# Optimization experiments

Measured on AMD Instinct MI355X. Metric: run time of the kernel, lower is better.

Reference implementation:

```python
import jax, jax.numpy as jnp
import numpy as np

NUM_EXPERTS = 8
TOP_K = 2
ROUTE_SCALE = 1.0
DIM = 1024
HID = 1024
B, S = 2, 4096


def setup_inputs() -> dict:
    key = jax.random.key(0)
    ks = jax.random.split(key, 9)
    sc = 0.05
    return {
        "x": jax.random.normal(ks[0], (B, S, DIM), dtype=jnp.float32),
        "gate_w": jax.random.normal(ks[1], (NUM_EXPERTS, DIM), dtype=jnp.float32) * sc,
        "w1": jax.random.normal(ks[2], (NUM_EXPERTS, HID, DIM), dtype=jnp.float32) * sc,
        "w2": jax.random.normal(ks[3], (NUM_EXPERTS, DIM, HID), dtype=jnp.float32) * sc,
        "w3": jax.random.normal(ks[4], (NUM_EXPERTS, HID, DIM), dtype=jnp.float32) * sc,
        "sw1": jax.random.normal(ks[5], (HID, DIM), dtype=jnp.float32) * sc,
        "sw2": jax.random.normal(ks[6], (DIM, HID), dtype=jnp.float32) * sc,
        "sw3": jax.random.normal(ks[7], (HID, DIM), dtype=jnp.float32) * sc,
        "expert_bias": jnp.zeros((NUM_EXPERTS,), dtype=jnp.float32),
    }


def reference(x, gate_w, w1, w2, w3, sw1, sw2, sw3, expert_bias):
    bs, slen, dim = x.shape
    xf = x.reshape(-1, dim)                      # [T, D]

    # ---- router (sigmoid scoring, top-k over scores + bias, gather true scores) ----
    scores = jax.nn.sigmoid((xf @ gate_w.T).astype(jnp.float32))   # [T, E]
    _, sel = jax.lax.top_k(scores + expert_bias[None, :], TOP_K)    # [T, K] int32
    top_scores = jnp.take_along_axis(scores, sel, axis=1) * ROUTE_SCALE  # [T, K]

    # ---- stable sort token-slots by chosen expert (dispatch permutation) ----
    flat_sel = sel.reshape(-1)                       # [T*K]
    order = jnp.argsort(flat_sel, stable=True)       # [T*K]
    scores_sorted = top_scores.reshape(-1)[order]    # [T*K]
    tok_idx = order // TOP_K                         # source token per slot
    expert_ids = flat_sel[order]                     # sorted expert id per slot

    routed = xf[tok_idx]                             # gather [T*K, D]
    # score_before_experts=True: scale inputs by routing score
    routed = (routed.astype(jnp.float32) * scores_sorted[:, None]).astype(x.dtype)

    # ---- grouped expert GLU MLP (loop over fixed expert count, masked) ----
    out_r = jnp.zeros_like(routed)
    for e in range(NUM_EXPERTS):
        m = (expert_ids == e)[:, None]
        h = jax.nn.silu(routed @ w1[e].T) * (routed @ w3[e].T)   # [T*K, H]
        out_r = out_r + jnp.where(m, h @ w2[e].T, jnp.zeros((), routed.dtype))

    # ---- shared expert on all tokens ----
    shared = (jax.nn.silu(xf @ sw1.T) * (xf @ sw3.T)) @ sw2.T    # [T, D]

    # NOTE: original code multiplies by routing scores again after experts
    # (in addition to score_before_experts) -- replicated faithfully.
    out_r = (out_r.astype(jnp.float32) * scores_sorted[:, None]).astype(x.dtype)

    out = shared.at[tok_idx].add(out_r)              # scatter-add combine
    return out.reshape(bs, slen, dim)
```

## Files before the change

### kernel.cpp

```cpp
#include <hip/hip_runtime.h>
#include <stdint.h>

typedef unsigned short u16;
typedef unsigned int u32;

#define T_TOK 8192
#define DIMSZ 1024
#define HIDSZ 1024
#define NE 8
#define NSLOT (T_TOK * 2)
#define NPAD (NSLOT + 1024)

typedef __attribute__((ext_vector_type(8))) __bf16 bf16x8;
typedef __attribute__((ext_vector_type(4))) float f32x4;

__device__ __forceinline__ size_t ablk(int pos, int c) {
  return ((((size_t)(pos >> 7) * 32 + (c >> 5)) * 4 + ((c >> 3) & 3)) * 128 +
          (pos & 127)) * 8 + (c & 7);
}

__device__ __forceinline__ u16 f2bf(float f) {
  u32 u = __builtin_bit_cast(u32, f);
  u += 0x7FFFu + ((u >> 16) & 1u);
  return (u16)(u >> 16);
}
__device__ __forceinline__ float bflo(u32 v) { return __builtin_bit_cast(float, v << 16); }
__device__ __forceinline__ float bfhi(u32 v) { return __builtin_bit_cast(float, v & 0xffff0000u); }
__device__ __forceinline__ u32 pack2(float a, float b) {
  return (u32)f2bf(a) | ((u32)f2bf(b) << 16);
}
__device__ __forceinline__ float silu_f(float v) { return v / (1.f + expf(-v)); }

__global__ __launch_bounds__(256) void convert_blocked(
    const float* __restrict__ s0, const float* __restrict__ s1,
    const float* __restrict__ s2, u16* __restrict__ d0, u16* __restrict__ d1,
    u16* __restrict__ d2) {
  const float* s = (blockIdx.y == 0) ? s0 : (blockIdx.y == 1) ? s1 : s2;
  u16* d = (blockIdx.y == 0) ? d0 : (blockIdx.y == 1) ? d1 : d2;
  __shared__ u16 lt[2048];
  int t = blockIdx.x;
  int rt = t >> 5, kt = t & 31;
  const float* sp = s + (size_t)rt * 64 * 1024 + kt * 32;
  int nl = threadIdx.x >> 2, k0 = (threadIdx.x & 3) * 8;
  float4 a = *(const float4*)(sp + (size_t)nl * 1024 + k0);
  float4 b = *(const float4*)(sp + (size_t)nl * 1024 + k0 + 4);
  uint4 p;
  p.x = pack2(a.x, a.y); p.y = pack2(a.z, a.w);
  p.z = pack2(b.x, b.y); p.w = pack2(b.z, b.w);
  *(uint4*)&lt[(threadIdx.x & 3) * 512 + nl * 8] = p;
  __syncthreads();
  *(uint4*)(d + (size_t)t * 2048 + threadIdx.x * 8) = *(const uint4*)&lt[threadIdx.x * 8];
}

__global__ __launch_bounds__(256) void router_kernel(
    const float* __restrict__ x, const float* __restrict__ gw,
    const float* __restrict__ bias, int* __restrict__ sel,
    float* __restrict__ selscore, u16* __restrict__ xb) {
  int t = blockIdx.x * 4 + (threadIdx.x >> 6);
  int lane = threadIdx.x & 63;
  float a[NE];
#pragma unroll
  for (int e = 0; e < NE; e++) a[e] = 0.f;
#pragma unroll
  for (int j = 0; j < 4; j++) {
    int c = j * 256 + lane * 4;
    float4 xv = *(const float4*)&x[(size_t)t * DIMSZ + c];
    uint2 p;
    p.x = pack2(xv.x, xv.y);
    p.y = pack2(xv.z, xv.w);
    *(uint2*)&xb[ablk(t, c)] = p;
#pragma unroll
    for (int e = 0; e < NE; e++) {
      float4 gv = *(const float4*)&gw[e * DIMSZ + c];
      a[e] = fmaf(xv.x, gv.x, fmaf(xv.y, gv.y, fmaf(xv.z, gv.z, fmaf(xv.w, gv.w, a[e]))));
    }
  }
#pragma unroll
  for (int off = 1; off < 64; off <<= 1)
#pragma unroll
    for (int e = 0; e < NE; e++) a[e] += __shfl_xor(a[e], off);
  if (lane == 0) {
    float s[NE], b[NE];
#pragma unroll
    for (int e = 0; e < NE; e++) {
      s[e] = 1.f / (1.f + expf(-a[e]));
      b[e] = s[e] + bias[e];
    }
    int e1 = 0; float v1 = b[0];
#pragma unroll
    for (int e = 1; e < NE; e++) if (b[e] > v1) { v1 = b[e]; e1 = e; }
    int e2 = -1; float v2 = -1e30f;
#pragma unroll
    for (int e = 0; e < NE; e++) if (e != e1 && b[e] > v2) { v2 = b[e]; e2 = e; }
    sel[t * 2] = e1; sel[t * 2 + 1] = e2;
    selscore[t * 2] = s[e1];
    selscore[t * 2 + 1] = s[e2];
  }
}

__global__ __launch_bounds__(1024) void rank_kernel(
    const int* __restrict__ sel, const float* __restrict__ selscore,
    int* __restrict__ slot2pos, float* __restrict__ slot_score,
    int* __restrict__ counts, int* __restrict__ offsets) {
  __shared__ int hist[NE * 1024];
  __shared__ int tot[NE];
  __shared__ int offs[NE];
  int tid = threadIdx.x;
  int sl[16];
  int h[NE];
#pragma unroll
  for (int e = 0; e < NE; e++) h[e] = 0;
#pragma unroll
  for (int j = 0; j < 4; j++) {
    int4 v = ((const int4*)sel)[tid * 4 + j];
    sl[j * 4 + 0] = v.x; sl[j * 4 + 1] = v.y;
    sl[j * 4 + 2] = v.z; sl[j * 4 + 3] = v.w;
  }
#pragma unroll
  for (int i = 0; i < 16; i++)
#pragma unroll
    for (int e = 0; e < NE; e++) h[e] += (sl[i] == e) ? 1 : 0;
#pragma unroll
  for (int e = 0; e < NE; e++) hist[e * 1024 + tid] = h[e];
  __syncthreads();
  int wid = tid >> 6, lane = tid & 63;
  if (wid < NE) {
    int e = wid;
    int vals[16];
    int lsum = 0;
#pragma unroll
    for (int i = 0; i < 16; i++) {
      int v = hist[e * 1024 + lane * 16 + i];
      vals[i] = lsum;
      lsum += v;
    }
    int incl = lsum;
#pragma unroll
    for (int off = 1; off < 64; off <<= 1) {
      int v = __shfl_up(incl, off);
      if (lane >= off) incl += v;
    }
    int excl = incl - lsum;
#pragma unroll
    for (int i = 0; i < 16; i++) hist[e * 1024 + lane * 16 + i] = vals[i] + excl;
    if (lane == 63) tot[e] = incl;
  }
  __syncthreads();
  if (tid == 0) {
    int acc = 0;
    for (int e = 0; e < NE; e++) {
      offs[e] = acc;
      offsets[e] = acc;
      counts[e] = tot[e];
      acc += (tot[e] + 127) & ~127;
    }
  }
  __syncthreads();
  int base[NE];
#pragma unroll
  for (int e = 0; e < NE; e++) base[e] = offs[e] + hist[e * 1024 + tid];
#pragma unroll
  for (int i = 0; i < 16; i++) {
    int slot = tid * 16 + i;
    int e = sl[i];
    int pos = 0;
#pragma unroll
    for (int k = 0; k < NE; k++) pos += (e == k) ? base[k] : 0;
#pragma unroll
    for (int k = 0; k < NE; k++) base[k] += (e == k) ? 1 : 0;
    slot2pos[slot] = pos;
    slot_score[pos] = selscore[slot];
  }
}

__global__ __launch_bounds__(256) void gather_kernel(
    const float* __restrict__ x, const float* __restrict__ selscore,
    const int* __restrict__ slot2pos, u16* __restrict__ routed) {
  int s = blockIdx.x * 4 + (threadIdx.x >> 6);
  int lane = threadIdx.x & 63;
  int pos = slot2pos[s];
  float sc = selscore[s];
  int t = s >> 1;
#pragma unroll
  for (int j = 0; j < 4; j++) {
    int c = j * 256 + lane * 4;
    float4 v = *(const float4*)&x[(size_t)t * DIMSZ + c];
    uint2 p;
    p.x = pack2(v.x * sc, v.y * sc);
    p.y = pack2(v.z * sc, v.w * sc);
    *(uint2*)&routed[ablk(pos, c)] = p;
  }
}

__global__ __launch_bounds__(256) void dual_glu_gemm(
    const u16* __restrict__ A, const u16* __restrict__ W1,
    const u16* __restrict__ W3, u16* __restrict__ Hout,
    const u16* __restrict__ As, const u16* __restrict__ SW1,
    const u16* __restrict__ SW3, u16* __restrict__ Hs,
    const int* __restrict__ seg_off, const int* __restrict__ seg_cnt) {
  int z = blockIdx.z;
  const u16 *Ap, *w1p, *w3p;
  u16* Hp;
  int soff, scnt;
  if (z < NE) {
    soff = seg_off[z]; scnt = seg_cnt[z];
    Ap = A;
    w1p = W1 + (size_t)z * HIDSZ * DIMSZ;
    w3p = W3 + (size_t)z * HIDSZ * DIMSZ;
    Hp = Hout;
  } else {
    soff = 0; scnt = T_TOK;
    Ap = As; w1p = SW1; w3p = SW3;
    Hp = Hs;
  }
  int mbase = blockIdx.y * 128;
  if (mbase >= scnt) return;
  int nbase = blockIdx.x * 64;

  __shared__ u16 lA[2][4096];
  __shared__ u16 lB1[2][2048];
  __shared__ u16 lB3[2][2048];

  int tid = threadIdx.x;
  int lane = tid & 63;
  int wid = tid >> 6;
  int wy = wid >> 1, wx = wid & 1;
  int q = lane >> 4, lm = lane & 15;

  f32x4 acc1[4][2], acc3[4][2];
#pragma unroll
  for (int i = 0; i < 4; i++)
#pragma unroll
    for (int j = 0; j < 2; j++) { acc1[i][j] = (f32x4)0.f; acc3[i][j] = (f32x4)0.f; }

  const u16* gA = Ap + ((size_t)((soff + mbase) >> 7) * 32) * 4096 + tid * 8;
  const u16* gB1 = w1p + ((size_t)(nbase >> 6) * 32) * 2048 + tid * 8;
  const u16* gB3 = w3p + ((size_t)(nbase >> 6) * 32) * 2048 + tid * 8;

  uint4 rA0 = *(const uint4*)gA;
  uint4 rA1 = *(const uint4*)(gA + 2048);
  uint4 rB1 = *(const uint4*)gB1;
  uint4 rB3 = *(const uint4*)gB3;
  gA += 4096; gB1 += 2048; gB3 += 2048;

  for (int kt = 0; kt < DIMSZ / 32; kt++) {
    int buf = kt & 1;
    *(uint4*)&lA[buf][tid * 8] = rA0;
    *(uint4*)&lA[buf][2048 + tid * 8] = rA1;
    *(uint4*)&lB1[buf][tid * 8] = rB1;
    *(uint4*)&lB3[buf][tid * 8] = rB3;
    __syncthreads();
    if (kt < DIMSZ / 32 - 1) {
      rA0 = *(const uint4*)gA;
      rA1 = *(const uint4*)(gA + 2048);
      rB1 = *(const uint4*)gB1;
      rB3 = *(const uint4*)gB3;
      gA += 4096; gB1 += 2048; gB3 += 2048;
    }
    bf16x8 af[4];
#pragma unroll
    for (int i = 0; i < 4; i++)
      af[i] = *(const bf16x8*)&lA[buf][(q * 128 + wy * 64 + i * 16 + lm) * 8];
    bf16x8 b1f[2], b3f[2];
#pragma unroll
    for (int j = 0; j < 2; j++) {
      int col = wx * 32 + j * 16 + lm;
      b1f[j] = *(const bf16x8*)&lB1[buf][(q * 64 + col) * 8];
      b3f[j] = *(const bf16x8*)&lB3[buf][(q * 64 + col) * 8];
    }
#pragma unroll
    for (int i = 0; i < 4; i++)
#pragma unroll
      for (int j = 0; j < 2; j++) {
        acc1[i][j] = __builtin_amdgcn_mfma_f32_16x16x32_bf16(af[i], b1f[j], acc1[i][j], 0, 0, 0);
        acc3[i][j] = __builtin_amdgcn_mfma_f32_16x16x32_bf16(af[i], b3f[j], acc3[i][j], 0, 0, 0);
      }
  }
#pragma unroll
  for (int i = 0; i < 4; i++) {
    int rowb = mbase + wy * 64 + i * 16 + q * 4;
#pragma unroll
    for (int j = 0; j < 2; j++) {
      int col = nbase + wx * 32 + j * 16 + lm;
      f32x4 g1 = acc1[i][j], g3 = acc3[i][j];
#pragma unroll
      for (int rr = 0; rr < 4; rr++) {
        int grow = rowb + rr;
        if (grow < scnt)
          Hp[ablk(soff + grow, col)] = f2bf(silu_f(g1[rr]) * g3[rr]);
      }
    }
  }
}

__global__ __launch_bounds__(256) void gemm2_kernel(
    const u16* __restrict__ A, const u16* __restrict__ W, u16* __restrict__ OutB,
    const u16* __restrict__ As, const u16* __restrict__ SW, float* __restrict__ OutF,
    const float* __restrict__ scale, const int* __restrict__ seg_off,
    const int* __restrict__ seg_cnt) {
  int z = blockIdx.z;
  const u16 *Ap, *wp;
  int soff, scnt;
  if (z < NE) {
    soff = seg_off[z]; scnt = seg_cnt[z];
    Ap = A; wp = W + (size_t)z * DIMSZ * HIDSZ;
  } else {
    soff = 0; scnt = T_TOK;
    Ap = As; wp = SW;
  }
  int mbase = blockIdx.y * 128;
  if (mbase >= scnt) return;
  int nbase = blockIdx.x * 128;

  __shared__ u16 lA[2][4096];
  __shared__ u16 lB[2][4096];

  int tid = threadIdx.x;
  int lane = tid & 63;
  int wid = tid >> 6;
  int wy = wid >> 1, wx = wid & 1;
  int q = lane >> 4, lm = lane & 15;

  f32x4 acc[4][4];
#pragma unroll
  for (int i = 0; i < 4; i++)
#pragma unroll
    for (int j = 0; j < 4; j++) acc[i][j] = (f32x4)0.f;

  const u16* gA = Ap + ((size_t)((soff + mbase) >> 7) * 32) * 4096 + tid * 8;
  const u16* gB0 = wp + ((size_t)(nbase >> 6) * 32) * 2048 + tid * 8;
  const u16* gB1 = wp + ((size_t)((nbase >> 6) + 1) * 32) * 2048 + tid * 8;

  uint4 rA0 = *(const uint4*)gA;
  uint4 rA1 = *(const uint4*)(gA + 2048);
  uint4 rB0 = *(const uint4*)gB0;
  uint4 rB1 = *(const uint4*)gB1;
  gA += 4096; gB0 += 2048; gB1 += 2048;

  for (int kt = 0; kt < HIDSZ / 32; kt++) {
    int buf = kt & 1;
    *(uint4*)&lA[buf][tid * 8] = rA0;
    *(uint4*)&lA[buf][2048 + tid * 8] = rA1;
    *(uint4*)&lB[buf][tid * 8] = rB0;
    *(uint4*)&lB[buf][2048 + tid * 8] = rB1;
    __syncthreads();
    if (kt < HIDSZ / 32 - 1) {
      rA0 = *(const uint4*)gA;
      rA1 = *(const uint4*)(gA + 2048);
      rB0 = *(const uint4*)gB0;
      rB1 = *(const uint4*)gB1;
      gA += 4096; gB0 += 2048; gB1 += 2048;
    }
    bf16x8 af[4], bf[4];
#pragma unroll
    for (int i = 0; i < 4; i++) {
      af[i] = *(const bf16x8*)&lA[buf][(q * 128 + wy * 64 + i * 16 + lm) * 8];
      bf[i] = *(const bf16x8*)&lB[buf][wx * 2048 + (q * 64 + i * 16 + lm) * 8];
    }
#pragma unroll
    for (int i = 0; i < 4; i++)
#pragma unroll
      for (int j = 0; j < 4; j++)
        acc[i][j] = __builtin_amdgcn_mfma_f32_16x16x32_bf16(af[i], bf[j], acc[i][j], 0, 0, 0);
  }
#pragma unroll
  for (int i = 0; i < 4; i++) {
    int rowb = mbase + wy * 64 + i * 16 + q * 4;
#pragma unroll
    for (int j = 0; j < 4; j++) {
      int col = nbase + wx * 64 + j * 16 + lm;
      f32x4 a = acc[i][j];
#pragma unroll
      for (int rr = 0; rr < 4; rr++) {
        int grow = rowb + rr;
        if (grow < scnt) {
          size_t idx = (size_t)(soff + grow) * DIMSZ + col;
          if (z < NE) {
            OutB[idx] = f2bf(a[rr] * scale[soff + grow]);
          } else {
            OutF[idx] = a[rr];
          }
        }
      }
    }
  }
}

__global__ __launch_bounds__(256) void combine_kernel(
    float* __restrict__ out, const u16* __restrict__ Orb,
    const int* __restrict__ slot2pos) {
  int t = blockIdx.x;
  int d = threadIdx.x * 4;
  int p0 = slot2pos[t * 2];
  int p1 = slot2pos[t * 2 + 1];
  float4 o = *(float4*)&out[(size_t)t * DIMSZ + d];
  uint2 a = *(const uint2*)&Orb[(size_t)p0 * DIMSZ + d];
  uint2 b = *(const uint2*)&Orb[(size_t)p1 * DIMSZ + d];
  o.x += bflo(a.x) + bflo(b.x);
  o.y += bfhi(a.x) + bfhi(b.x);
  o.z += bflo(a.y) + bflo(b.y);
  o.w += bfhi(a.y) + bfhi(b.y);
  *(float4*)&out[(size_t)t * DIMSZ + d] = o;
}

extern "C" void kernel_launch(void* const* d_in, const int* in_sizes, int n_in,
                              void* d_out, int out_size, void* d_ws, size_t ws_size,
                              hipStream_t stream) {
  const float* x = (const float*)d_in[0];
  const float* gw = (const float*)d_in[1];
  const float* w1 = (const float*)d_in[2];
  const float* w2 = (const float*)d_in[3];
  const float* w3 = (const float*)d_in[4];
  const float* sw1 = (const float*)d_in[5];
  const float* sw2 = (const float*)d_in[6];
  const float* sw3 = (const float*)d_in[7];
  const float* bias = (const float*)d_in[8];
  float* out = (float*)d_out;

  uint8_t* ws = (uint8_t*)d_ws;
  size_t off = 0;
  auto alloc = [&](size_t b) { size_t o = off; off += (b + 255) & ~(size_t)255; return o; };

  size_t ctrl = alloc(256);
  int* counts = (int*)(ws + ctrl);
  int* offsets = counts + 16;
  int* sel = (int*)(ws + alloc((size_t)NSLOT * 4));
  float* selscore = (float*)(ws + alloc((size_t)NSLOT * 4));
  float* slot_score = (float*)(ws + alloc((size_t)NPAD * 4));
  int* slot2pos = (int*)(ws + alloc((size_t)NSLOT * 4));
  u16* xb = (u16*)(ws + alloc((size_t)T_TOK * DIMSZ * 2));
  u16* routed = (u16*)(ws + alloc((size_t)NPAD * DIMSZ * 2));
  u16* Hbuf = (u16*)(ws + alloc((size_t)NPAD * HIDSZ * 2));
  u16* Orb = (u16*)(ws + alloc((size_t)NPAD * DIMSZ * 2));
  u16* Hs = (u16*)(ws + alloc((size_t)T_TOK * HIDSZ * 2));
  u16* w1b = (u16*)(ws + alloc((size_t)NE * HIDSZ * DIMSZ * 2));
  u16* w2b = (u16*)(ws + alloc((size_t)NE * DIMSZ * HIDSZ * 2));
  u16* w3b = (u16*)(ws + alloc((size_t)NE * HIDSZ * DIMSZ * 2));
  u16* sw1b = (u16*)(ws + alloc((size_t)HIDSZ * DIMSZ * 2));
  u16* sw2b = (u16*)(ws + alloc((size_t)DIMSZ * HIDSZ * 2));
  u16* sw3b = (u16*)(ws + alloc((size_t)HIDSZ * DIMSZ * 2));

  convert_blocked<<<dim3(NE * 16 * 32, 3), 256, 0, stream>>>(
      w1, w2, w3, w1b, w2b, w3b);
  convert_blocked<<<dim3(16 * 32, 3), 256, 0, stream>>>(
      sw1, sw2, sw3, sw1b, sw2b, sw3b);

  router_kernel<<<T_TOK / 4, 256, 0, stream>>>(x, gw, bias, sel, selscore, xb);
  rank_kernel<<<1, 1024, 0, stream>>>(sel, selscore, slot2pos, slot_score,
                                      counts, offsets);
  gather_kernel<<<NSLOT / 4, 256, 0, stream>>>(x, selscore, slot2pos, routed);

  dual_glu_gemm<<<dim3(16, 64, NE + 1), 256, 0, stream>>>(
      routed, w1b, w3b, Hbuf, xb, sw1b, sw3b, Hs, offsets, counts);
  gemm2_kernel<<<dim3(8, 64, NE + 1), 256, 0, stream>>>(
      Hbuf, w2b, Orb, Hs, sw2b, out, slot_score, offsets, counts);

  combine_kernel<<<T_TOK, 256, 0, stream>>>(out, Orb, slot2pos);
}
```

Measured before the change: 524.7 us.

## Switch expert GEMMs to 32x32x16 MFMA with manual double-buffer unroll

```diff
diff --git a/kernel.cpp b/kernel.cpp
--- a/kernel.cpp
+++ b/kernel.cpp
@@ -12,7 +12,9 @@
 #define NPAD (NSLOT + 1024)
 
 typedef __attribute__((ext_vector_type(8))) __bf16 bf16x8;
-typedef __attribute__((ext_vector_type(4))) float f32x4;
+typedef __attribute__((ext_vector_type(16))) float f32x16;
+
+#define MFMA32(a, b, c) __builtin_amdgcn_mfma_f32_32x32x16_bf16(a, b, c, 0, 0, 0)
 
 __device__ __forceinline__ size_t ablk(int pos, int c) {
   return ((((size_t)(pos >> 7) * 32 + (c >> 5)) * 4 + ((c >> 3) & 3)) * 128 +
@@ -33,12 +35,22 @@
 
 __global__ __launch_bounds__(256) void convert_blocked(
     const float* __restrict__ s0, const float* __restrict__ s1,
-    const float* __restrict__ s2, u16* __restrict__ d0, u16* __restrict__ d1,
-    u16* __restrict__ d2) {
-  const float* s = (blockIdx.y == 0) ? s0 : (blockIdx.y == 1) ? s1 : s2;
-  u16* d = (blockIdx.y == 0) ? d0 : (blockIdx.y == 1) ? d1 : d2;
+    const float* __restrict__ s2, const float* __restrict__ ss0,
+    const float* __restrict__ ss1, const float* __restrict__ ss2,
+    u16* __restrict__ d0, u16* __restrict__ d1, u16* __restrict__ d2,
+    u16* __restrict__ ds0, u16* __restrict__ ds1, u16* __restrict__ ds2) {
   __shared__ u16 lt[2048];
   int t = blockIdx.x;
+  const float* s;
+  u16* d;
+  if (t < NE * 16 * 32) {
+    s = (blockIdx.y == 0) ? s0 : (blockIdx.y == 1) ? s1 : s2;
+    d = (blockIdx.y == 0) ? d0 : (blockIdx.y == 1) ? d1 : d2;
+  } else {
+    t -= NE * 16 * 32;
+    s = (blockIdx.y == 0) ? ss0 : (blockIdx.y == 1) ? ss1 : ss2;
+    d = (blockIdx.y == 0) ? ds0 : (blockIdx.y == 1) ? ds1 : ds2;
+  }
   int rt = t >> 5, kt = t & 31;
   const float* sp = s + (size_t)rt * 64 * 1024 + kt * 32;
   int nl = threadIdx.x >> 2, k0 = (threadIdx.x & 3) * 8;
@@ -192,7 +204,7 @@
   }
 }
 
-__global__ __launch_bounds__(256) void dual_glu_gemm(
+__global__ __launch_bounds__(256, 3) void dual_glu_gemm(
     const u16* __restrict__ A, const u16* __restrict__ W1,
     const u16* __restrict__ W3, u16* __restrict__ Hout,
     const u16* __restrict__ As, const u16* __restrict__ SW1,
@@ -225,13 +237,13 @@
   int lane = tid & 63;
   int wid = tid >> 6;
   int wy = wid >> 1, wx = wid & 1;
-  int q = lane >> 4, lm = lane & 15;
-
-  f32x4 acc1[4][2], acc3[4][2];
-#pragma unroll
-  for (int i = 0; i < 4; i++)
-#pragma unroll
-    for (int j = 0; j < 2; j++) { acc1[i][j] = (f32x4)0.f; acc3[i][j] = (f32x4)0.f; }
+  int l5 = lane >> 5, l31 = lane & 31;
+  int aoff = (l5 * 128 + wy * 64 + l31) * 8;
+  int boff = (l5 * 64 + wx * 32 + l31) * 8;
+
+  f32x16 acc1[2], acc3[2];
+  acc1[0] = (f32x16)0.f; acc1[1] = (f32x16)0.f;
+  acc3[0] = (f32x16)0.f; acc3[1] = (f32x16)0.f;
 
   const u16* gA = Ap + ((size_t)((soff + mbase) >> 7) * 32) * 4096 + tid * 8;
   const u16* gB1 = w1p + ((size_t)(nbase >> 6) * 32) * 2048 + tid * 8;
@@ -243,57 +255,57 @@
   uint4 rB3 = *(const uint4*)gB3;
   gA += 4096; gB1 += 2048; gB3 += 2048;
 
-  for (int kt = 0; kt < DIMSZ / 32; kt++) {
-    int buf = kt & 1;
-    *(uint4*)&lA[buf][tid * 8] = rA0;
-    *(uint4*)&lA[buf][2048 + tid * 8] = rA1;
-    *(uint4*)&lB1[buf][tid * 8] = rB1;
-    *(uint4*)&lB3[buf][tid * 8] = rB3;
+#define DG_STAGE(B)                                                   \
+  *(uint4*)&lA[B][tid * 8] = rA0;                                     \
+  *(uint4*)&lA[B][2048 + tid * 8] = rA1;                              \
+  *(uint4*)&lB1[B][tid * 8] = rB1;                                    \
+  *(uint4*)&lB3[B][tid * 8] = rB3;
+
+#define DG_LOAD()                                                     \
+  rA0 = *(const uint4*)gA;                                            \
+  rA1 = *(const uint4*)(gA + 2048);                                   \
+  rB1 = *(const uint4*)gB1;                                           \
+  rB3 = *(const uint4*)gB3;                                           \
+  gA += 4096; gB1 += 2048; gB3 += 2048;
+
+#define DG_COMPUTE(B)                                                 \
+  _Pragma("unroll")                                                   \
+  for (int s = 0; s < 2; s++) {                                       \
+    bf16x8 a0 = *(const bf16x8*)&lA[B][aoff + s * 2048];              \
+    bf16x8 a1 = *(const bf16x8*)&lA[B][aoff + s * 2048 + 256];        \
+    bf16x8 b1 = *(const bf16x8*)&lB1[B][boff + s * 1024];             \
+    bf16x8 b3 = *(const bf16x8*)&lB3[B][boff + s * 1024];             \
+    acc1[0] = MFMA32(a0, b1, acc1[0]);                                \
+    acc3[0] = MFMA32(a0, b3, acc3[0]);                                \
+    acc1[1] = MFMA32(a1, b1, acc1[1]);                                \
+    acc3[1] = MFMA32(a1, b3, acc3[1]);                                \
+  }
+
+  for (int kt = 0; kt < 32; kt += 2) {
+    DG_STAGE(0);
     __syncthreads();
-    if (kt < DIMSZ / 32 - 1) {
-      rA0 = *(const uint4*)gA;
-      rA1 = *(const uint4*)(gA + 2048);
-      rB1 = *(const uint4*)gB1;
-      rB3 = *(const uint4*)gB3;
-      gA += 4096; gB1 += 2048; gB3 += 2048;
-    }
-    bf16x8 af[4];
-#pragma unroll
-    for (int i = 0; i < 4; i++)
-      af[i] = *(const bf16x8*)&lA[buf][(q * 128 + wy * 64 + i * 16 + lm) * 8];
-    bf16x8 b1f[2], b3f[2];
-#pragma unroll
-    for (int j = 0; j < 2; j++) {
-      int col = wx * 32 + j * 16 + lm;
-      b1f[j] = *(const bf16x8*)&lB1[buf][(q * 64 + col) * 8];
-      b3f[j] = *(const bf16x8*)&lB3[buf][(q * 64 + col) * 8];
-    }
-#pragma unroll
-    for (int i = 0; i < 4; i++)
-#pragma unroll
-      for (int j = 0; j < 2; j++) {
-        acc1[i][j] = __builtin_amdgcn_mfma_f32_16x16x32_bf16(af[i], b1f[j], acc1[i][j], 0, 0, 0);
-        acc3[i][j] = __builtin_amdgcn_mfma_f32_16x16x32_bf16(af[i], b3f[j], acc3[i][j], 0, 0, 0);
-      }
-  }
-#pragma unroll
-  for (int i = 0; i < 4; i++) {
-    int rowb = mbase + wy * 64 + i * 16 + q * 4;
-#pragma unroll
-    for (int j = 0; j < 2; j++) {
-      int col = nbase + wx * 32 + j * 16 + lm;
-      f32x4 g1 = acc1[i][j], g3 = acc3[i][j];
-#pragma unroll
-      for (int rr = 0; rr < 4; rr++) {
-        int grow = rowb + rr;
-        if (grow < scnt)
-          Hp[ablk(soff + grow, col)] = f2bf(silu_f(g1[rr]) * g3[rr]);
-      }
-    }
-  }
-}
-
-__global__ __launch_bounds__(256) void gemm2_kernel(
+    DG_LOAD();
+    DG_COMPUTE(0);
+    DG_STAGE(1);
+    __syncthreads();
+    if (kt < 30) { DG_LOAD(); }
+    DG_COMPUTE(1);
+  }
+
+#pragma unroll
+  for (int i = 0; i < 2; i++) {
+    int colg = nbase + wx * 32 + l31;
+#pragma unroll
+    for (int r = 0; r < 16; r++) {
+      int rowl = (r & 3) + 8 * (r >> 2) + 4 * l5;
+      int grow = mbase + wy * 64 + i * 32 + rowl;
+      if (grow < scnt)
+        Hp[ablk(soff + grow, colg)] = f2bf(silu_f(acc1[i][r]) * acc3[i][r]);
+    }
+  }
+}
+
+__global__ __launch_bounds__(256, 3) void gemm2_kernel(
     const u16* __restrict__ A, const u16* __restrict__ W, u16* __restrict__ OutB,
     const u16* __restrict__ As, const u16* __restrict__ SW, float* __restrict__ OutF,
     const float* __restrict__ scale, const int* __restrict__ seg_off,
@@ -319,13 +331,13 @@
   int lane = tid & 63;
   int wid = tid >> 6;
   int wy = wid >> 1, wx = wid & 1;
-  int q = lane >> 4, lm = lane & 15;
-
-  f32x4 acc[4][4];
-#pragma unroll
-  for (int i = 0; i < 4; i++)
-#pragma unroll
-    for (int j = 0; j < 4; j++) acc[i][j] = (f32x4)0.f;
+  int l5 = lane >> 5, l31 = lane & 31;
+  int aoff = (l5 * 128 + wy * 64 + l31) * 8;
+  int boff = wx * 2048 + (l5 * 64 + l31) * 8;
+
+  f32x16 acc[2][2];
+  acc[0][0] = (f32x16)0.f; acc[0][1] = (f32x16)0.f;
+  acc[1][0] = (f32x16)0.f; acc[1][1] = (f32x16)0.f;
 
   const u16* gA = Ap + ((size_t)((soff + mbase) >> 7) * 32) * 4096 + tid * 8;
   const u16* gB0 = wp + ((size_t)(nbase >> 6) * 32) * 2048 + tid * 8;
@@ -337,48 +349,58 @@
   uint4 rB1 = *(const uint4*)gB1;
   gA += 4096; gB0 += 2048; gB1 += 2048;
 
-  for (int kt = 0; kt < HIDSZ / 32; kt++) {
-    int buf = kt & 1;
-    *(uint4*)&lA[buf][tid * 8] = rA0;
-    *(uint4*)&lA[buf][2048 + tid * 8] = rA1;
-    *(uint4*)&lB[buf][tid * 8] = rB0;
-    *(uint4*)&lB[buf][2048 + tid * 8] = rB1;
+#define G2_STAGE(B)                                                   \
+  *(uint4*)&lA[B][tid * 8] = rA0;                                     \
+  *(uint4*)&lA[B][2048 + tid * 8] = rA1;                              \
+  *(uint4*)&lB[B][tid * 8] = rB0;                                     \
+  *(uint4*)&lB[B][2048 + tid * 8] = rB1;
+
+#define G2_LOAD()                                                     \
+  rA0 = *(const uint4*)gA;                                            \
+  rA1 = *(const uint4*)(gA + 2048);                                   \
+  rB0 = *(const uint4*)gB0;                                           \
+  rB1 = *(const uint4*)gB1;                                           \
+  gA += 4096; gB0 += 2048; gB1 += 2048;
+
+#define G2_COMPUTE(B)                                                 \
+  _Pragma("unroll")                                                   \
+  for (int s = 0; s < 2; s++) {                                       \
+    bf16x8 a0 = *(const bf16x8*)&lA[B][aoff + s * 2048];              \
+    bf16x8 a1 = *(const bf16x8*)&lA[B][aoff + s * 2048 + 256];        \
+    bf16x8 b0 = *(const bf16x8*)&lB[B][boff + s * 1024];              \
+    bf16x8 b1 = *(const bf16x8*)&lB[B][boff + s * 1024 + 256];        \
+    acc[0][0] = MFMA32(a0, b0, acc[0][0]);                            \
+    acc[0][1] = MFMA32(a0, b1, acc[0][1]);                            \
+    acc[1][0] = MFMA32(a1, b0, acc[1][0]);                            \
+    acc[1][1] = MFMA32(a1, b1, acc[1][1]);                            \
+  }
+
+  for (int kt = 0; kt < 32; kt += 2) {
+    G2_STAGE(0);
     __syncthreads();
-    if (kt < HIDSZ / 32 - 1) {
-      rA0 = *(const uint4*)gA;
-      rA1 = *(const uint4*)(gA + 2048);
-      rB0 = *(const uint4*)gB0;
-      rB1 = *(const uint4*)gB1;
-      gA += 4096; gB0 += 2048; gB1 += 2048;
-    }
-    bf16x8 af[4], bf[4];
-#pragma unroll
-    for (int i = 0; i < 4; i++) {
-      af[i] = *(const bf16x8*)&lA[buf][(q * 128 + wy * 64 + i * 16 + lm) * 8];
-      bf[i] = *(const bf16x8*)&lB[buf][wx * 2048 + (q * 64 + i * 16 + lm) * 8];
-    }
-#pragma unroll
-    for (int i = 0; i < 4; i++)
-#pragma unroll
-      for (int j = 0; j < 4; j++)
-        acc[i][j] = __builtin_amdgcn_mfma_f32_16x16x32_bf16(af[i], bf[j], acc[i][j], 0, 0, 0);
-  }
-#pragma unroll
-  for (int i = 0; i < 4; i++) {
-    int rowb = mbase + wy * 64 + i * 16 + q * 4;
-#pragma unroll
-    for (int j = 0; j < 4; j++) {
-      int col = nbase + wx * 64 + j * 16 + lm;
-      f32x4 a = acc[i][j];
-#pragma unroll
-      for (int rr = 0; rr < 4; rr++) {
-        int grow = rowb + rr;
+    G2_LOAD();
+    G2_COMPUTE(0);
+    G2_STAGE(1);
+    __syncthreads();
+    if (kt < 30) { G2_LOAD(); }
+    G2_COMPUTE(1);
+  }
+
+#pragma unroll
+  for (int i = 0; i < 2; i++) {
+#pragma unroll
+    for (int j = 0; j < 2; j++) {
+      int colg = nbase + wx * 64 + j * 32 + l31;
+#pragma unroll
+      for (int r = 0; r < 16; r++) {
+        int rowl = (r & 3) + 8 * (r >> 2) + 4 * l5;
+        int grow = mbase + wy * 64 + i * 32 + rowl;
         if (grow < scnt) {
-          size_t idx = (size_t)(soff + grow) * DIMSZ + col;
+          size_t idx = (size_t)(soff + grow) * DIMSZ + colg;
           if (z < NE) {
-            OutB[idx] = f2bf(a[rr] * scale[soff + grow]);
+            OutB[idx] = f2bf(acc[i][j][r] * scale[soff + grow]);
           } else {
-            OutF[idx] = a[rr];
+            OutF[idx] = acc[i][j][r];
           }
         }
       }
@@ -440,10 +462,8 @@
   u16* sw2b = (u16*)(ws + alloc((size_t)DIMSZ * HIDSZ * 2));
   u16* sw3b = (u16*)(ws + alloc((size_t)HIDSZ * DIMSZ * 2));
 
-  convert_blocked<<<dim3(NE * 16 * 32, 3), 256, 0, stream>>>(
-      w1, w2, w3, w1b, w2b, w3b);
-  convert_blocked<<<dim3(16 * 32, 3), 256, 0, stream>>>(
-      sw1, sw2, sw3, sw1b, sw2b, sw3b);
+  convert_blocked<<<dim3((NE + 1) * 16 * 32, 3), 256, 0, stream>>>(
+      w1, w2, w3, sw1, sw2, sw3, w1b, w2b, w3b, sw1b, sw2b, sw3b);
 
   router_kernel<<<T_TOK / 4, 256, 0, stream>>>(x, gw, bias, sel, selscore, xb);
   rank_kernel<<<1, 1024, 0, stream>>>(sel, selscore, slot2pos, slot_score,
```

After: 495.6 us. -5.6%, faster.
